# Performance work log

Measured on AMD Instinct MI355X. Metric: run time of the kernel, lower is better.

The kernel has to match this reference:

```python
import jax, jax.numpy as jnp
import numpy as np

D_MODEL = 1024
HEADS = 16
D_K = D_MODEL // HEADS
B, S = 2, 2048
NEG = -1000000000.0

def setup_inputs() -> dict:
    key = jax.random.key(0)
    ks = jax.random.split(key, 11)
    sc = 1.0 / np.sqrt(D_MODEL)
    inp = {
        'q': jax.random.normal(ks[0], (B, S, D_MODEL), jnp.float32),
        'k': jax.random.normal(ks[1], (B, S, D_MODEL), jnp.float32),
        'v': jax.random.normal(ks[2], (B, S, D_MODEL), jnp.float32),
        'mask': jnp.tril(jnp.ones((S, S), jnp.int32))[None, None],  # causal [1,1,S,S]
        'wq_w': jax.random.normal(ks[3], (D_MODEL, D_MODEL), jnp.float32) * sc,
        'wq_b': jax.random.normal(ks[4], (D_MODEL,), jnp.float32) * 0.02,
        'wk_w': jax.random.normal(ks[5], (D_MODEL, D_MODEL), jnp.float32) * sc,
        'wk_b': jax.random.normal(ks[6], (D_MODEL,), jnp.float32) * 0.02,
        'wv_w': jax.random.normal(ks[7], (D_MODEL, D_MODEL), jnp.float32) * sc,
        'wv_b': jax.random.normal(ks[8], (D_MODEL,), jnp.float32) * 0.02,
        'wo_w': jax.random.normal(ks[9], (D_MODEL, D_MODEL), jnp.float32) * sc,
        'wo_b': jax.random.normal(ks[10], (D_MODEL,), jnp.float32) * 0.02,
    }
    return inp

def reference(q, k, v, mask, wq_w, wq_b, wk_w, wk_b, wv_w, wv_b, wo_w, wo_b):
    b, s, _ = q.shape
    # projections (torch Linear: x @ W^T + b)
    Q = (q @ wq_w.T + wq_b).reshape(b, s, HEADS, D_K).transpose(0, 2, 1, 3)  # [B,H,S,Dk]
    K = (k @ wk_w.T + wk_b).reshape(b, s, HEADS, D_K).transpose(0, 2, 1, 3)
    V = (v @ wv_w.T + wv_b).reshape(b, s, HEADS, D_K).transpose(0, 2, 1, 3)
    scores = jnp.einsum('bhqd,bhkd->bhqk', Q, K) / jnp.sqrt(jnp.float32(D_K))
    scores = jnp.where(mask == 0, NEG, scores)
    p = jax.nn.softmax(scores, axis=-1)  # dropout=0.0 -> identity
    x = jnp.einsum('bhqk,bhkd->bhqd', p, V)
    x = x.transpose(0, 2, 1, 3).reshape(b, s, D_MODEL)
    return x @ wo_w.T + wo_b
```

## Files before the change

kernel.cpp:

```cpp
#include <hip/hip_runtime.h>

typedef unsigned short u16;
typedef __attribute__((ext_vector_type(8))) short bf16x8;
typedef __attribute__((ext_vector_type(4))) float f32x4;

#define SEQ 2048
#define DMODEL 1024

__device__ __forceinline__ u16 f2bf(float f) {
    union { float f; unsigned u; } x; x.f = f;
    unsigned r = x.u + 0x7fffu + ((x.u >> 16) & 1u);
    return (u16)(r >> 16);
}

__device__ __forceinline__ u16 f2bf_trunc(float f) {
    union { float f; unsigned u; } x; x.f = f;
    return (u16)(x.u >> 16);
}

__device__ __forceinline__ float bf2f(u16 v) {
    union { unsigned u; float f; } x; x.u = ((unsigned)v) << 16;
    return x.f;
}

__device__ __forceinline__ f32x4 mfma16(bf16x8 a, bf16x8 b, f32x4 c) {
    return __builtin_amdgcn_mfma_f32_16x16x32_bf16(a, b, c, 0, 0, 0);
}

__device__ __forceinline__ void gld16(const u16* g, u16* l) {
    __builtin_amdgcn_global_load_lds(
        (__attribute__((address_space(1))) const void*)g,
        (__attribute__((address_space(3))) void*)l, 16, 0, 0);
}

struct CvtArgs {
    const float* src[7];
    u16* dst[7];
    int n4[7];
};

__global__ __launch_bounds__(256) void cvt_kernel(CvtArgs a) {
    const int id = blockIdx.y;
    const int i = blockIdx.x * 256 + threadIdx.x;
    if (i >= a.n4[id]) return;
    float4 f = ((const float4*)a.src[id])[i];
    ushort4 u;
    u.x = f2bf(f.x); u.y = f2bf(f.y); u.z = f2bf(f.z); u.w = f2bf(f.w);
    ((ushort4*)a.dst[id])[i] = u;
}


__global__ __launch_bounds__(256, 4) void gemm_qkv(
    const u16* __restrict__ Xq, const u16* __restrict__ Xk, const u16* __restrict__ Xv,
    const u16* __restrict__ Wq, const u16* __restrict__ Wk, const u16* __restrict__ Wv,
    const float* __restrict__ bq, const float* __restrict__ bk, const float* __restrict__ bv,
    u16* __restrict__ Qb, u16* __restrict__ Kb, u16* __restrict__ Vb)
{
    __shared__ u16 Abuf[2][128 * 32];
    __shared__ u16 Bbuf[2][128 * 32];

    const int bid = blockIdx.x;
    const int gm = (bid & 7) * 96 + (bid >> 3);
    const int z = gm >> 8;
    const int rem = gm & 255;
    const int bm = (rem >> 3) * 128;
    const int bn = (rem & 7) * 128;

    const u16* X = (z == 0) ? Xq : (z == 1) ? Xk : Xv;
    const u16* W = (z == 0) ? Wq : (z == 1) ? Wk : Wv;
    const float* bias = (z == 0) ? bq : (z == 1) ? bk : bv;

    const int tid = threadIdx.x;
    const int lane = tid & 63, w = tid >> 6;
    const int wm = (w >> 1) * 64, wn = (w & 1) * 64;
    const int r = lane & 15, qd = lane >> 4;

    const int srow = lane >> 2;
    const int scol = (lane & 3) * 8;
    const u16* Xs = X + (size_t)(bm + w * 32 + srow) * 1024 + scol;
    const u16* Ws = W + (size_t)(bn + w * 32 + srow) * 1024 + scol;

    f32x4 acc[4][4];
    #pragma unroll
    for (int i = 0; i < 4; ++i)
        #pragma unroll
        for (int j = 0; j < 4; ++j)
            acc[i][j] = (f32x4){0.f, 0.f, 0.f, 0.f};

    auto stage = [&](int t) {
        const int d = t & 1;
        #pragma unroll
        for (int q = 0; q < 2; ++q) {
            gld16(Xs + (size_t)q * 16384 + t * 32, &Abuf[d][w * 1024 + q * 512]);
            gld16(Ws + (size_t)q * 16384 + t * 32, &Bbuf[d][w * 1024 + q * 512]);
        }
    };

    stage(0);
    stage(1);
    asm volatile("s_waitcnt vmcnt(4)" ::: "memory");
    __builtin_amdgcn_sched_barrier(0);
    __builtin_amdgcn_s_barrier();

    for (int t = 0; t < 32; ++t) {
        const u16* Ab = Abuf[t & 1];
        const u16* Bb = Bbuf[t & 1];
        bf16x8 aF[4], bF[4];
        #pragma unroll
        for (int i = 0; i < 4; ++i)
            aF[i] = *(const bf16x8*)(Ab + (wm + i * 16 + r) * 32 + qd * 8);
        #pragma unroll
        for (int j = 0; j < 4; ++j)
            bF[j] = *(const bf16x8*)(Bb + (wn + j * 16 + r) * 32 + qd * 8);
        __builtin_amdgcn_s_setprio(1);
        #pragma unroll
        for (int i = 0; i < 4; ++i)
            #pragma unroll
            for (int j = 0; j < 4; ++j)
                acc[i][j] = mfma16(aF[i], bF[j], acc[i][j]);
        __builtin_amdgcn_s_setprio(0);
        if (t == 31) break;
        asm volatile("s_waitcnt lgkmcnt(0)" ::: "memory");
        __builtin_amdgcn_sched_barrier(0);
        __builtin_amdgcn_s_barrier();
        if (t < 30) {
            stage(t + 2);
            asm volatile("s_waitcnt vmcnt(4)" ::: "memory");
        } else {
            asm volatile("s_waitcnt vmcnt(0)" ::: "memory");
        }
        __builtin_amdgcn_sched_barrier(0);
        __builtin_amdgcn_s_barrier();
        __builtin_amdgcn_sched_barrier(0);
    }

    const float scale = (z == 0) ? 0.18033688011112042f : 1.0f;
    #pragma unroll
    for (int j = 0; j < 4; ++j) {
        const int n = bn + wn + j * 16 + r;
        const float bvl = bias[n];
        const int h = n >> 6, d = n & 63;
        #pragma unroll
        for (int i = 0; i < 4; ++i) {
            const int m0 = bm + wm + i * 16 + qd * 4;
            const int b_ = m0 >> 11, s0 = m0 & 2047;
            if (z == 0) {
                #pragma unroll
                for (int reg = 0; reg < 4; ++reg)
                    Qb[(size_t)(m0 + reg) * 1024 + n] = f2bf((acc[i][j][reg] + bvl) * scale);
            } else if (z == 1) {
                #pragma unroll
                for (int reg = 0; reg < 4; ++reg)
                    Kb[((size_t)(b_ * 16 + h) * SEQ + s0 + reg) * 64 + d] =
                        f2bf(acc[i][j][reg] + bvl);
            } else {
                ushort4 u;
                u.x = f2bf(acc[i][j][0] + bvl);
                u.y = f2bf(acc[i][j][1] + bvl);
                u.z = f2bf(acc[i][j][2] + bvl);
                u.w = f2bf(acc[i][j][3] + bvl);
                *(ushort4*)(Vb + ((size_t)(b_ * 16 + h) * 64 + d) * SEQ + s0) = u;
            }
        }
    }
}

__global__ __launch_bounds__(256, 4) void attn_kernel(
    const u16* __restrict__ Qb, const u16* __restrict__ Kb,
    const u16* __restrict__ Vb, u16* __restrict__ Op, float* __restrict__ Lp)
{
    __shared__ u16 Kst[2][4096];
    __shared__ u16 Vst[2][4096];
    __shared__ u16 Pst[4][16 * 64];

    const int bid = blockIdx.x;
    const int xcd = bid & 7;
    const int i2 = bid >> 3;
    const int bh = xcd + 8 * (i2 & 3);
    const int rest = i2 >> 2;
    const int gidx = rest / 3;
    const int third = rest - gidx * 3;
    const int g = 31 - gidx;
    const int b_ = bh >> 4, h = bh & 15;

    const int n = g + 1;
    const int j0 = (n * third) / 3;
    const int j1 = (n * (third + 1)) / 3;

    const int tid = threadIdx.x;
    const int lane = tid & 63, w = tid >> 6;
    const int r = lane & 15, qd = lane >> 4;

    const u16* Kh = Kb + (size_t)bh * SEQ * 64;
    const u16* Vh = Vb + (size_t)bh * 64 * SEQ;
    u16* Pw = Pst[w];

    bf16x8 aQ[2];
    {
        const size_t qoff =
            (size_t)(b_ * SEQ + g * 64 + w * 16 + r) * DMODEL + h * 64;
        aQ[0] = *(const bf16x8*)(Qb + qoff + qd * 8);
        aQ[1] = *(const bf16x8*)(Qb + qoff + 32 + qd * 8);
    }

    bf16x8 ones;
    #pragma unroll
    for (int e = 0; e < 8; ++e) ones[e] = (short)0x3F80;

    f32x4 o[4];
    f32x4 l = (f32x4){0.f, 0.f, 0.f, 0.f};
    #pragma unroll
    for (int db = 0; db < 4; ++db) o[db] = (f32x4){0.f, 0.f, 0.f, 0.f};

    auto stage = [&](int j, int buf) {
        if (w < 2) {
            const u16* Kt = Kh + (size_t)j * 64 * 64;
            #pragma unroll
            for (int s = 0; s < 4; ++s) {
                const int ss = w * 4 + s;
                gld16(Kt + ((ss >> 1) * 16 + r) * 64 + (ss & 1) * 32 + qd * 8,
                      &Kst[buf][ss * 512]);
            }
        } else {
            const u16* Vt = Vh + j * 64;
            #pragma unroll
            for (int s = 0; s < 4; ++s) {
                const int ss = (w - 2) * 4 + s;
                gld16(Vt + (size_t)((ss >> 1) * 16 + r) * SEQ + (ss & 1) * 32 + qd * 8,
                      &Vst[buf][ss * 512]);
            }
        }
    };

    if (j0 < j1) stage(j0, j0 & 1);

    const f32x4 shift = (f32x4){-23.083120654223414f, -23.083120654223414f,
                                -23.083120654223414f, -23.083120654223414f};

    const int rx = r & 7;

    for (int j = j0; j < j1; ++j) {
        const int cur = j & 1;
        __syncthreads();
        if (j + 1 < j1) stage(j + 1, 1 - cur);

        bf16x8 kf[4][2], vf[4][2];
        #pragma unroll
        for (int nb = 0; nb < 4; ++nb) {
            kf[nb][0] = *(const bf16x8*)(&Kst[cur][(nb * 2 + 0) * 512 + lane * 8]);
            kf[nb][1] = *(const bf16x8*)(&Kst[cur][(nb * 2 + 1) * 512 + lane * 8]);
        }
        #pragma unroll
        for (int db = 0; db < 4; ++db) {
            vf[db][0] = *(const bf16x8*)(&Vst[cur][(db * 2 + 0) * 512 + lane * 8]);
            vf[db][1] = *(const bf16x8*)(&Vst[cur][(db * 2 + 1) * 512 + lane * 8]);
        }

        f32x4 sc[4];
        #pragma unroll
        for (int nb = 0; nb < 4; ++nb) {
            f32x4 s = shift;
            s = mfma16(kf[nb][0], aQ[0], s);
            s = mfma16(kf[nb][1], aQ[1], s);
            sc[nb] = s;
        }

        if (j == g) {
            const int rowr = w * 16 + r;
            #pragma unroll
            for (int nb = 0; nb < 4; ++nb)
                #pragma unroll
                for (int reg = 0; reg < 4; ++reg)
                    if (nb * 16 + qd * 4 + reg > rowr) sc[nb][reg] = -1e30f;
        }

        #pragma unroll
        for (int nb = 0; nb < 4; ++nb)
            #pragma unroll
            for (int reg = 0; reg < 4; ++reg)
                sc[nb][reg] = exp2f(sc[nb][reg]);

        #pragma unroll
        for (int nb = 0; nb < 4; ++nb) {
            ushort4 pk;
            pk.x = f2bf_trunc(sc[nb][0]);
            pk.y = f2bf_trunc(sc[nb][1]);
            pk.z = f2bf_trunc(sc[nb][2]);
            pk.w = f2bf_trunc(sc[nb][3]);
            const int gw = (nb * 2 + (qd >> 1)) ^ rx;
            *(ushort4*)(Pw + r * 64 + gw * 8 + (qd & 1) * 4) = pk;
        }

        const bf16x8 aP0 = *(const bf16x8*)(Pw + r * 64 + ((qd ^ rx) * 8));
        const bf16x8 aP1 = *(const bf16x8*)(Pw + r * 64 + (((4 + qd) ^ rx) * 8));

        l = mfma16(aP0, ones, l);
        l = mfma16(aP1, ones, l);

        #pragma unroll
        for (int db = 0; db < 4; ++db) {
            o[db] = mfma16(aP0, vf[db][0], o[db]);
            o[db] = mfma16(aP1, vf[db][1], o[db]);
        }
    }

    u16* Oh = Op + ((size_t)(third * 1024 + bh * 32 + g) * 4096);
    float* Lh = Lp + (size_t)(third * 1024 + bh * 32 + g) * 64;
    #pragma unroll
    for (int db = 0; db < 4; ++db)
        #pragma unroll
        for (int reg = 0; reg < 4; ++reg)
            Oh[(w * 16 + qd * 4 + reg) * 64 + db * 16 + r] = f2bf(o[db][reg]);
    if (r == 0) {
        #pragma unroll
        for (int reg = 0; reg < 4; ++reg)
            Lh[w * 16 + qd * 4 + reg] = l[reg];
    }
}

__global__ __launch_bounds__(256) void attn_norm(
    const u16* __restrict__ Op, const float* __restrict__ Lp,
    u16* __restrict__ AO)
{
    const int idx = blockIdx.x * 256 + threadIdx.x;
    const int col8 = idx & 127;
    const int row = idx >> 7;
    const int h = col8 >> 3;
    const int b_ = row >> 11, s = row & 2047;
    const int g = s >> 6, r64 = s & 63;
    const int bh = b_ * 16 + h;

    const size_t pa = ((size_t)(bh * 32 + g) * 4096) + r64 * 64 + (col8 & 7) * 8;
    const size_t pb = pa + (size_t)1024 * 4096;
    const size_t pc = pb + (size_t)1024 * 4096;
    const float la = Lp[(bh * 32 + g) * 64 + r64];
    const float lb = Lp[(1024 + bh * 32 + g) * 64 + r64];
    const float lc = Lp[(2048 + bh * 32 + g) * 64 + r64];
    const float inv = 1.0f / (la + lb + lc);

    const bf16x8 a = *(const bf16x8*)(Op + pa);
    const bf16x8 b = *(const bf16x8*)(Op + pb);
    const bf16x8 c = *(const bf16x8*)(Op + pc);
    bf16x8 o;
    #pragma unroll
    for (int e = 0; e < 8; ++e)
        o[e] = (short)f2bf((bf2f((u16)a[e]) + bf2f((u16)b[e]) + bf2f((u16)c[e])) * inv);
    *(bf16x8*)(AO + (size_t)row * 1024 + col8 * 8) = o;
}

__global__ __launch_bounds__(256, 4) void gemm_out(
    const u16* __restrict__ AO, const u16* __restrict__ W,
    const float* __restrict__ bias, float* __restrict__ out)
{
    __shared__ u16 Abuf[2][64 * 32];
    __shared__ u16 Bbuf[2][128 * 32];

    const int bid = blockIdx.x;
    const int gm = (bid & 7) * 64 + (bid >> 3);
    const int bm = (gm >> 3) * 64;
    const int bn = (gm & 7) * 128;

    const int tid = threadIdx.x;
    const int lane = tid & 63, w = tid >> 6;
    const int wm = (w >> 1) * 32, wn = (w & 1) * 64;
    const int r = lane & 15, qd = lane >> 4;

    const int srow = lane >> 2;
    const int scol = (lane & 3) * 8;
    const u16* Xs = AO + (size_t)(bm + w * 16 + srow) * 1024 + scol;
    const u16* Ws = W + (size_t)(bn + w * 32 + srow) * 1024 + scol;

    f32x4 acc[2][4];
    #pragma unroll
    for (int i = 0; i < 2; ++i)
        #pragma unroll
        for (int j = 0; j < 4; ++j)
            acc[i][j] = (f32x4){0.f, 0.f, 0.f, 0.f};

    auto stage = [&](int t) {
        const int d = t & 1;
        gld16(Xs + t * 32, &Abuf[d][w * 512]);
        #pragma unroll
        for (int q = 0; q < 2; ++q)
            gld16(Ws + (size_t)q * 16384 + t * 32, &Bbuf[d][w * 1024 + q * 512]);
    };

    stage(0);
    stage(1);
    asm volatile("s_waitcnt vmcnt(3)" ::: "memory");
    __builtin_amdgcn_sched_barrier(0);
    __builtin_amdgcn_s_barrier();

    for (int t = 0; t < 32; ++t) {
        const u16* Ab = Abuf[t & 1];
        const u16* Bb = Bbuf[t & 1];
        bf16x8 aF[2], bF[4];
        #pragma unroll
        for (int i = 0; i < 2; ++i)
            aF[i] = *(const bf16x8*)(Ab + (wm + i * 16 + r) * 32 + qd * 8);
        #pragma unroll
        for (int j = 0; j < 4; ++j)
            bF[j] = *(const bf16x8*)(Bb + (wn + j * 16 + r) * 32 + qd * 8);
        __builtin_amdgcn_s_setprio(1);
        #pragma unroll
        for (int i = 0; i < 2; ++i)
            #pragma unroll
            for (int j = 0; j < 4; ++j)
                acc[i][j] = mfma16(aF[i], bF[j], acc[i][j]);
        __builtin_amdgcn_s_setprio(0);
        if (t == 31) break;
        asm volatile("s_waitcnt lgkmcnt(0)" ::: "memory");
        __builtin_amdgcn_sched_barrier(0);
        __builtin_amdgcn_s_barrier();
        if (t < 30) {
            stage(t + 2);
            asm volatile("s_waitcnt vmcnt(3)" ::: "memory");
        } else {
            asm volatile("s_waitcnt vmcnt(0)" ::: "memory");
        }
        __builtin_amdgcn_sched_barrier(0);
        __builtin_amdgcn_s_barrier();
        __builtin_amdgcn_sched_barrier(0);
    }

    #pragma unroll
    for (int j = 0; j < 4; ++j) {
        const int n = bn + wn + j * 16 + r;
        const float bvl = bias[n];
        #pragma unroll
        for (int i = 0; i < 2; ++i) {
            const int m0 = bm + wm + i * 16 + qd * 4;
            #pragma unroll
            for (int reg = 0; reg < 4; ++reg)
                out[(size_t)(m0 + reg) * 1024 + n] = acc[i][j][reg] + bvl;
        }
    }
}

extern "C" void kernel_launch(void* const* d_in, const int* in_sizes, int n_in,
                              void* d_out, int out_size, void* d_ws, size_t ws_size,
                              hipStream_t stream) {
    const float* q  = (const float*)d_in[0];
    const float* k  = (const float*)d_in[1];
    const float* v  = (const float*)d_in[2];
    const float* wq = (const float*)d_in[4];
    const float* bq = (const float*)d_in[5];
    const float* wk = (const float*)d_in[6];
    const float* bk = (const float*)d_in[7];
    const float* wv = (const float*)d_in[8];
    const float* bv = (const float*)d_in[9];
    const float* wo = (const float*)d_in[10];
    const float* bo = (const float*)d_in[11];
    float* out = (float*)d_out;

    u16* ws = (u16*)d_ws;
    u16* Xq = ws;
    u16* Xk = Xq + (size_t)4194304;
    u16* Xv = Xk + (size_t)4194304;
    u16* Wq = Xv + (size_t)4194304;
    u16* Wk = Wq + (size_t)1048576;
    u16* Wv = Wk + (size_t)1048576;
    u16* Wo = Wv + (size_t)1048576;
    u16* Qb = Wo + (size_t)1048576;
    u16* Kb = Qb + (size_t)4194304;
    u16* Vb = Kb + (size_t)4194304;
    u16* AO = Vb + (size_t)4194304;

    u16* Op = ws;
    float* Lp = (float*)(ws + (size_t)12582912);

    CvtArgs ca;
    ca.src[0] = q;  ca.dst[0] = Xq; ca.n4[0] = 1048576;
    ca.src[1] = k;  ca.dst[1] = Xk; ca.n4[1] = 1048576;
    ca.src[2] = v;  ca.dst[2] = Xv; ca.n4[2] = 1048576;
    ca.src[3] = wq; ca.dst[3] = Wq; ca.n4[3] = 262144;
    ca.src[4] = wk; ca.dst[4] = Wk; ca.n4[4] = 262144;
    ca.src[5] = wv; ca.dst[5] = Wv; ca.n4[5] = 262144;
    ca.src[6] = wo; ca.dst[6] = Wo; ca.n4[6] = 262144;

    cvt_kernel<<<dim3(4096, 7), 256, 0, stream>>>(ca);
    gemm_qkv<<<dim3(768), 256, 0, stream>>>(Xq, Xk, Xv, Wq, Wk, Wv,
                                            bq, bk, bv, Qb, Kb, Vb);
    attn_kernel<<<dim3(3072), 256, 0, stream>>>(Qb, Kb, Vb, Op, Lp);
    attn_norm<<<dim3(2048), 256, 0, stream>>>(Op, Lp, AO);
    gemm_out<<<dim3(512), 256, 0, stream>>>(AO, Wo, bo, out);
}
```

Measured before the change: 234.0 us.

## Process 128 query rows per attention block to reuse staged K/V tiles

```diff
diff --git a/kernel.cpp b/kernel.cpp
--- a/kernel.cpp
+++ b/kernel.cpp
@@ -48,7 +48,6 @@
     u.x = f2bf(f.x); u.y = f2bf(f.y); u.z = f2bf(f.z); u.w = f2bf(f.w);
     ((ushort4*)a.dst[id])[i] = u;
 }
-
 
 __global__ __launch_bounds__(256, 4) void gemm_qkv(
     const u16* __restrict__ Xq, const u16* __restrict__ Xk, const u16* __restrict__ Xv,
@@ -178,12 +177,12 @@
     const int i2 = bid >> 3;
     const int bh = xcd + 8 * (i2 & 3);
     const int rest = i2 >> 2;
-    const int gidx = rest / 3;
-    const int third = rest - gidx * 3;
-    const int g = 31 - gidx;
+    const int gpidx = rest / 3;
+    const int third = rest - gpidx * 3;
+    const int gp = 15 - gpidx;
     const int b_ = bh >> 4, h = bh & 15;
 
-    const int n = g + 1;
+    const int n = 2 * gp + 2;
     const int j0 = (n * third) / 3;
     const int j1 = (n * (third + 1)) / 3;
 
@@ -195,22 +194,27 @@
     const u16* Vh = Vb + (size_t)bh * 64 * SEQ;
     u16* Pw = Pst[w];
 
-    bf16x8 aQ[2];
-    {
+    bf16x8 aQ[2][2];
+    #pragma unroll
+    for (int i = 0; i < 2; ++i) {
         const size_t qoff =
-            (size_t)(b_ * SEQ + g * 64 + w * 16 + r) * DMODEL + h * 64;
-        aQ[0] = *(const bf16x8*)(Qb + qoff + qd * 8);
-        aQ[1] = *(const bf16x8*)(Qb + qoff + 32 + qd * 8);
+            (size_t)(b_ * SEQ + gp * 128 + w * 32 + i * 16 + r) * DMODEL + h * 64;
+        aQ[i][0] = *(const bf16x8*)(Qb + qoff + qd * 8);
+        aQ[i][1] = *(const bf16x8*)(Qb + qoff + 32 + qd * 8);
     }
 
     bf16x8 ones;
     #pragma unroll
     for (int e = 0; e < 8; ++e) ones[e] = (short)0x3F80;
 
-    f32x4 o[4];
-    f32x4 l = (f32x4){0.f, 0.f, 0.f, 0.f};
-    #pragma unroll
-    for (int db = 0; db < 4; ++db) o[db] = (f32x4){0.f, 0.f, 0.f, 0.f};
+    f32x4 o[2][4];
+    f32x4 l[2];
+    #pragma unroll
+    for (int i = 0; i < 2; ++i) {
+        l[i] = (f32x4){0.f, 0.f, 0.f, 0.f};
+        #pragma unroll
+        for (int db = 0; db < 4; ++db) o[i][db] = (f32x4){0.f, 0.f, 0.f, 0.f};
+    }
 
     auto stage = [&](int j, int buf) {
         if (w < 2) {
@@ -236,7 +240,6 @@
 
     const f32x4 shift = (f32x4){-23.083120654223414f, -23.083120654223414f,
                                 -23.083120654223414f, -23.083120654223414f};
-
     const int rx = r & 7;
 
     for (int j = j0; j < j1; ++j) {
@@ -256,65 +259,72 @@
             vf[db][1] = *(const bf16x8*)(&Vst[cur][(db * 2 + 1) * 512 + lane * 8]);
         }
 
-        f32x4 sc[4];
-        #pragma unroll
-        for (int nb = 0; nb < 4; ++nb) {
-            f32x4 s = shift;
-            s = mfma16(kf[nb][0], aQ[0], s);
-            s = mfma16(kf[nb][1], aQ[1], s);
-            sc[nb] = s;
-        }
-
-        if (j == g) {
-            const int rowr = w * 16 + r;
+        #pragma unroll
+        for (int i = 0; i < 2; ++i) {
+            f32x4 sc[4];
+            #pragma unroll
+            for (int nb = 0; nb < 4; ++nb) {
+                f32x4 s = shift;
+                s = mfma16(kf[nb][0], aQ[i][0], s);
+                s = mfma16(kf[nb][1], aQ[i][1], s);
+                sc[nb] = s;
+            }
+
+            if (j >= 2 * gp) {
+                const int lim = gp * 128 + w * 32 + i * 16 + r - j * 64;
+                #pragma unroll
+                for (int nb = 0; nb < 4; ++nb)
+                    #pragma unroll
+                    for (int reg = 0; reg < 4; ++reg)
+                        if (nb * 16 + qd * 4 + reg > lim) sc[nb][reg] = -1e30f;
+            }
+
             #pragma unroll
             for (int nb = 0; nb < 4; ++nb)
                 #pragma unroll
                 for (int reg = 0; reg < 4; ++reg)
-                    if (nb * 16 + qd * 4 + reg > rowr) sc[nb][reg] = -1e30f;
-        }
-
-        #pragma unroll
-        for (int nb = 0; nb < 4; ++nb)
+                    sc[nb][reg] = exp2f(sc[nb][reg]);
+
+            #pragma unroll
+            for (int nb = 0; nb < 4; ++nb) {
+                ushort4 pk;
+                pk.x = f2bf_trunc(sc[nb][0]);
+                pk.y = f2bf_trunc(sc[nb][1]);
+                pk.z = f2bf_trunc(sc[nb][2]);
+                pk.w = f2bf_trunc(sc[nb][3]);
+                const int gw = (nb * 2 + (qd >> 1)) ^ rx;
+                *(ushort4*)(Pw + r * 64 + gw * 8 + (qd & 1) * 4) = pk;
+            }
+
+            const bf16x8 aP0 = *(const bf16x8*)(Pw + r * 64 + ((qd ^ rx) * 8));
+            const bf16x8 aP1 = *(const bf16x8*)(Pw + r * 64 + (((4 + qd) ^ rx) * 8));
+
+            l[i] = mfma16(aP0, ones, l[i]);
+            l[i] = mfma16(aP1, ones, l[i]);
+
+            #pragma unroll
+            for (int db = 0; db < 4; ++db) {
+                o[i][db] = mfma16(aP0, vf[db][0], o[i][db]);
+                o[i][db] = mfma16(aP1, vf[db][1], o[i][db]);
+            }
+        }
+    }
+
+    u16* Oh = Op + ((size_t)(third * 1024 + bh * 32 + gp * 2) * 4096);
+    float* Lh = Lp + (size_t)(third * 1024 + bh * 32 + gp * 2) * 64;
+    #pragma unroll
+    for (int i = 0; i < 2; ++i) {
+        #pragma unroll
+        for (int db = 0; db < 4; ++db)
             #pragma unroll
             for (int reg = 0; reg < 4; ++reg)
-                sc[nb][reg] = exp2f(sc[nb][reg]);
-
-        #pragma unroll
-        for (int nb = 0; nb < 4; ++nb) {
-            ushort4 pk;
-            pk.x = f2bf_trunc(sc[nb][0]);
-            pk.y = f2bf_trunc(sc[nb][1]);
-            pk.z = f2bf_trunc(sc[nb][2]);
-            pk.w = f2bf_trunc(sc[nb][3]);
-            const int gw = (nb * 2 + (qd >> 1)) ^ rx;
-            *(ushort4*)(Pw + r * 64 + gw * 8 + (qd & 1) * 4) = pk;
-        }
-
-        const bf16x8 aP0 = *(const bf16x8*)(Pw + r * 64 + ((qd ^ rx) * 8));
-        const bf16x8 aP1 = *(const bf16x8*)(Pw + r * 64 + (((4 + qd) ^ rx) * 8));
-
-        l = mfma16(aP0, ones, l);
-        l = mfma16(aP1, ones, l);
-
-        #pragma unroll
-        for (int db = 0; db < 4; ++db) {
-            o[db] = mfma16(aP0, vf[db][0], o[db]);
-            o[db] = mfma16(aP1, vf[db][1], o[db]);
-        }
-    }
-
-    u16* Oh = Op + ((size_t)(third * 1024 + bh * 32 + g) * 4096);
-    float* Lh = Lp + (size_t)(third * 1024 + bh * 32 + g) * 64;
-    #pragma unroll
-    for (int db = 0; db < 4; ++db)
-        #pragma unroll
-        for (int reg = 0; reg < 4; ++reg)
-            Oh[(w * 16 + qd * 4 + reg) * 64 + db * 16 + r] = f2bf(o[db][reg]);
-    if (r == 0) {
-        #pragma unroll
-        for (int reg = 0; reg < 4; ++reg)
-            Lh[w * 16 + qd * 4 + reg] = l[reg];
+                Oh[(w * 32 + i * 16 + qd * 4 + reg) * 64 + db * 16 + r] =
+                    f2bf(o[i][db][reg]);
+        if (r == 0) {
+            #pragma unroll
+            for (int reg = 0; reg < 4; ++reg)
+                Lh[w * 32 + i * 16 + qd * 4 + reg] = l[i][reg];
+        }
     }
 }
 
@@ -481,7 +491,7 @@
     cvt_kernel<<<dim3(4096, 7), 256, 0, stream>>>(ca);
     gemm_qkv<<<dim3(768), 256, 0, stream>>>(Xq, Xk, Xv, Wq, Wk, Wv,
                                             bq, bk, bv, Qb, Kb, Vb);
-    attn_kernel<<<dim3(3072), 256, 0, stream>>>(Qb, Kb, Vb, Op, Lp);
+    attn_kernel<<<dim3(1536), 256, 0, stream>>>(Qb, Kb, Vb, Op, Lp);
     attn_norm<<<dim3(2048), 256, 0, stream>>>(Op, Lp, AO);
     gemm_out<<<dim3(512), 256, 0, stream>>>(AO, Wo, bo, out);
 }
```

Measured after the change: 339.8 us. 45.2% more time.
